# Optimization experiments

Measured on AMD Instinct MI355X. Metric: run time of the kernel, lower is better.

## Reference

```python
import jax, jax.numpy as jnp
import numpy as np

B, N_OBJ, N_REL = 32, 100, 512
D_OBJ, D_CTX, D_HID = 1024, 1024, 1024


def setup_inputs() -> dict:
    key = jax.random.key(0)
    k1, k2, k3, k4, k5 = jax.random.split(key, 5)
    object_branch_output = jax.random.normal(k1, (B * N_OBJ, D_OBJ), dtype=jnp.float32)
    context_branch_output = jax.random.normal(k2, (B, D_CTX), dtype=jnp.float32)
    num_obj = jnp.full((B,), N_OBJ, dtype=jnp.int32)
    num_rels = jnp.full((B,), N_REL, dtype=jnp.int32)
    obj_pairs = jax.random.randint(k3, (B, N_REL, 2), 0, N_OBJ, dtype=jnp.int32)
    W1 = jax.random.normal(k4, (D_OBJ + D_CTX, D_HID), dtype=jnp.float32) * (1.0 / np.sqrt(D_OBJ + D_CTX))
    b1 = jnp.zeros((D_HID,), dtype=jnp.float32)
    W2 = jax.random.normal(k5, (D_HID, D_HID), dtype=jnp.float32) * (1.0 / np.sqrt(D_HID))
    b2 = jnp.zeros((D_HID,), dtype=jnp.float32)
    return {
        "object_branch_output": object_branch_output,
        "context_branch_output": context_branch_output,
        "num_obj": num_obj,
        "num_rels": num_rels,
        "obj_pairs": obj_pairs,
        "W1": W1, "b1": b1, "W2": W2, "b2": b2,
    }


def reference(object_branch_output, context_branch_output, num_obj, num_rels,
              obj_pairs, W1, b1, W2, b2):
    # --- prepare_f_oo_vis_input, fully vectorized ---
    # per-batch object index offsets: sum(num_obj[:b])  (exclusive cumsum)
    obj_offsets = jnp.cumsum(num_obj) - num_obj                       # [B]
    global_pairs = obj_pairs + obj_offsets[:, None, None]             # [B, R, 2]
    # gather both endpoints of every pair and mean-aggregate
    pair_feats = object_branch_output[global_pairs]                   # [B, R, 2, D_obj]
    obj_vec = pair_feats.mean(axis=2)                                 # [B, R, D_obj]
    # broadcast per-batch context vector to every relation, then concat
    ctx = jnp.broadcast_to(context_branch_output[:, None, :],
                           obj_vec.shape[:2] + (context_branch_output.shape[-1],))
    input_f_oo_vis = jnp.concatenate([obj_vec, ctx], axis=-1)         # [B, R, D_obj+D_ctx]
    x = input_f_oo_vis.reshape(-1, input_f_oo_vis.shape[-1])          # [tot_rels, D_obj+D_ctx]
    # --- f_oo_vis MLP: (Linear -> ReLU) per layer pair ---
    h = jax.nn.relu(x @ W1 + b1)
    f_oo_vis_output = jax.nn.relu(h @ W2 + b2)
    return object_branch_output, f_oo_vis_output
```

## Files before the change

### kernel.cpp

```cpp
#include <hip/hip_runtime.h>
#include <hip/hip_bf16.h>

#define BB   32
#define NREL 512
#define DD   1024
#define MTOT (BB * NREL)
#define OBJ_ROWS (BB * 100)

typedef __attribute__((ext_vector_type(8))) short bf16x8;
typedef __attribute__((ext_vector_type(4))) float f32x4;

__device__ __forceinline__ unsigned short f2bf(float f) {
    union { float f; unsigned u; } v; v.f = f;
    unsigned r = v.u + 0x7fff + ((v.u >> 16) & 1);
    return (unsigned short)(r >> 16);
}

__device__ __forceinline__ void gld16(const void* g, void* l) {
    __builtin_amdgcn_global_load_lds(
        (const __attribute__((address_space(1))) unsigned int*)g,
        (__attribute__((address_space(3))) unsigned int*)l,
        16, 0, 0);
}

__device__ __forceinline__ void barfence() {
    asm volatile("" ::: "memory");
    __builtin_amdgcn_s_barrier();
    asm volatile("" ::: "memory");
}

__global__ void __launch_bounds__(256) prep_kernel(
    const float* __restrict__ obj, const float* __restrict__ ctx,
    const int* __restrict__ num_obj, const int* __restrict__ pairs,
    const float* __restrict__ W1, const float* __restrict__ W2,
    unsigned short* __restrict__ W1t, unsigned short* __restrict__ W2t,
    float* __restrict__ part, unsigned short* __restrict__ objvec,
    float* __restrict__ out_obj) {
    __shared__ float smem[32 * 33];
    int bid = blockIdx.x;
    int tid = threadIdx.x;

    if (bid < 1024) {
        int slice = bid & 3, chunk = (bid >> 2) & 7, b = bid >> 5;
        int nl = tid & 127, kh = tid >> 7;
        int n = chunk * 128 + nl;
        int kbase = slice * 256 + kh * 128;
        const float* c = ctx + (size_t)b * DD + kbase;
        const float* w = W1 + (size_t)(DD + kbase) * DD + n;
        float a0 = 0.f, a1 = 0.f, a2 = 0.f, a3 = 0.f;
#pragma unroll 8
        for (int k = 0; k < 128; k += 4) {
            a0 = fmaf(c[k + 0], w[(size_t)(k + 0) * DD], a0);
            a1 = fmaf(c[k + 1], w[(size_t)(k + 1) * DD], a1);
            a2 = fmaf(c[k + 2], w[(size_t)(k + 2) * DD], a2);
            a3 = fmaf(c[k + 3], w[(size_t)(k + 3) * DD], a3);
        }
        smem[kh * 128 + nl] = (a0 + a1) + (a2 + a3);
        __syncthreads();
        if (kh == 0)
            part[(((size_t)slice * BB + b) << 10) + n] = smem[nl] + smem[128 + nl];
    } else if (bid < 3072) {
        const float* W = (bid < 2048) ? W1 : W2;
        unsigned short* Wt = (bid < 2048) ? W1t : W2t;
        int t = (bid - 1024) & 1023;
        int k0 = (t >> 5) * 32, n0 = (t & 31) * 32;
        int tr = tid >> 5, tc = tid & 31;
#pragma unroll
        for (int i = 0; i < 4; i++)
            smem[(tr + i * 8) * 33 + tc] = W[(size_t)(k0 + tr + i * 8) * DD + n0 + tc];
        __syncthreads();
#pragma unroll
        for (int i = 0; i < 4; i++)
            Wt[(size_t)(n0 + tr + i * 8) * DD + k0 + tc] = f2bf(smem[tc * 33 + tr + i * 8]);
    } else if (bid < 7168) {
        int rbase = (bid - 3072) * 4;
        int b = rbase >> 9;
        int off = 0;
        for (int i = 0; i < b; i++) off += num_obj[i];
#pragma unroll
        for (int rr = 0; rr < 4; rr++) {
            int row = rbase + rr;
            int i0 = pairs[2 * row] + off;
            int i1 = pairs[2 * row + 1] + off;
            float4 x = ((const float4*)obj)[(size_t)i0 * (DD / 4) + tid];
            float4 y = ((const float4*)obj)[(size_t)i1 * (DD / 4) + tid];
            ushort4 o;
            o.x = f2bf(0.5f * (x.x + y.x));
            o.y = f2bf(0.5f * (x.y + y.y));
            o.z = f2bf(0.5f * (x.z + y.z));
            o.w = f2bf(0.5f * (x.w + y.w));
            ((ushort4*)(objvec + (size_t)row * DD))[tid] = o;
        }
    } else {
        const float4* src = (const float4*)obj;
        float4* dst = (float4*)out_obj;
        for (int i = (bid - 7168) * 256 + tid; i < OBJ_ROWS * DD / 4; i += 2048 * 256)
            dst[i] = src[i];
    }
}

template <int MODE>
__global__ void __launch_bounds__(512, 2) gemm256_kernel(
    const unsigned short* __restrict__ A,
    const unsigned short* __restrict__ Bt,
    const float* __restrict__ bias,
    const float* __restrict__ bias2,
    void* __restrict__ Cout) {
    constexpr int K = 1024;
    constexpr int NT = K / 64;
    extern __shared__ unsigned short lds[];
    int tid = threadIdx.x;
    int lane = tid & 63, wave = tid >> 6;
    int wr = wave >> 2, wc = wave & 3;
    int lr = lane & 15, g = lane >> 4;

    int wg = blockIdx.x;
    int swz = (wg & 7) * 32 + (wg >> 3);
    int mBase = (swz >> 2) * 256;
    int nBase = (swz & 3) * 256;

    const unsigned short* Ab = A + (size_t)mBase * K;
    const unsigned short* Bb = Bt + (size_t)nBase * K;

    int srow[4], soff[4], sdst[4];
#pragma unroll
    for (int i = 0; i < 4; i++) {
        int s = i * 512 + tid;
        int row = s >> 3, cperm = s & 7;
        srow[i] = row;
        soff[i] = (cperm ^ (row & 7)) * 8;
        sdst[i] = s * 8;
    }

    f32x4 acc[8][4];
#pragma unroll
    for (int i = 0; i < 8; i++)
#pragma unroll
        for (int j = 0; j < 4; j++) acc[i][j] = (f32x4){0.f, 0.f, 0.f, 0.f};

    auto STAGE = [&](int bi, int kt) {
        unsigned short* Ad = lds + bi * 16384;
        unsigned short* Bd = lds + 32768 + bi * 16384;
        int ko = kt * 64;
#pragma unroll
        for (int i = 0; i < 4; i++) {
            gld16(Ab + (size_t)srow[i] * K + ko + soff[i], Ad + sdst[i]);
            gld16(Bb + (size_t)srow[i] * K + ko + soff[i], Bd + sdst[i]);
        }
    };

    auto COMPUTE = [&](int bi) {
        const unsigned short* As = lds + bi * 16384;
        const unsigned short* Bs = lds + 32768 + bi * 16384;
        bf16x8 bfr[4][2];
#pragma unroll
        for (int n = 0; n < 4; n++)
#pragma unroll
            for (int kk = 0; kk < 2; kk++) {
                int row = wc * 64 + n * 16 + lr;
                int c = kk * 4 + g;
                bfr[n][kk] = *(const bf16x8*)&Bs[row * 64 + ((c ^ (row & 7)) * 8)];
            }
#pragma unroll
        for (int half = 0; half < 2; half++) {
            bf16x8 af[4][2];
#pragma unroll
            for (int m = 0; m < 4; m++)
#pragma unroll
                for (int kk = 0; kk < 2; kk++) {
                    int row = wr * 128 + (half * 4 + m) * 16 + lr;
                    int c = kk * 4 + g;
                    af[m][kk] = *(const bf16x8*)&As[row * 64 + ((c ^ (row & 7)) * 8)];
                }
            __builtin_amdgcn_s_setprio(1);
#pragma unroll
            for (int m = 0; m < 4; m++)
#pragma unroll
                for (int n = 0; n < 4; n++)
#pragma unroll
                    for (int kk = 0; kk < 2; kk++)
                        acc[half * 4 + m][n] = __builtin_amdgcn_mfma_f32_16x16x32_bf16(
                            af[m][kk], bfr[n][kk], acc[half * 4 + m][n], 0, 0, 0);
            __builtin_amdgcn_s_setprio(0);
        }
    };

    STAGE(0, 0);
    int cur = 0;
    for (int kt = 0; kt < NT - 1; ++kt) {
        STAGE(cur ^ 1, kt + 1);
        asm volatile("s_waitcnt vmcnt(8)" ::: "memory");
        barfence();
        COMPUTE(cur);
        barfence();
        cur ^= 1;
    }
    asm volatile("s_waitcnt vmcnt(0)" ::: "memory");
    barfence();
    COMPUTE(cur);

    int rg = g * 4;
    int bb = mBase >> 9;
#pragma unroll
    for (int m = 0; m < 8; m++) {
#pragma unroll
        for (int n = 0; n < 4; n++) {
            int col = nBase + wc * 64 + n * 16 + lr;
            float bv;
            if (MODE == 1) {
                bv = bias2[col];
#pragma unroll
                for (int s = 0; s < 4; s++)
                    bv += bias[(((size_t)s * BB + bb) << 10) + col];
            } else {
                bv = bias[col];
            }
#pragma unroll
            for (int r = 0; r < 4; r++) {
                int row = mBase + wr * 128 + m * 16 + rg + r;
                float v = acc[m][n][r] + bv;
                v = v > 0.f ? v : 0.f;
                if (MODE == 1)
                    ((unsigned short*)Cout)[(size_t)row * 1024 + col] = f2bf(v);
                else
                    ((float*)Cout)[(size_t)row * 1024 + col] = v;
            }
        }
    }
}

extern "C" void kernel_launch(void* const* d_in, const int* in_sizes, int n_in,
                              void* d_out, int out_size, void* d_ws, size_t ws_size,
                              hipStream_t stream) {
    (void)in_sizes; (void)n_in; (void)out_size; (void)ws_size;
    const float* obj     = (const float*)d_in[0];
    const float* ctx     = (const float*)d_in[1];
    const int*   num_obj = (const int*)d_in[2];
    const int*   pairs   = (const int*)d_in[4];
    const float* W1      = (const float*)d_in[5];
    const float* b1      = (const float*)d_in[6];
    const float* W2      = (const float*)d_in[7];
    const float* b2      = (const float*)d_in[8];

    char* ws = (char*)d_ws;
    unsigned short* objvec = (unsigned short*)(ws);
    unsigned short* h      = (unsigned short*)(ws + 33554432);
    unsigned short* W1t    = (unsigned short*)(ws + 67108864);
    unsigned short* W2t    = (unsigned short*)(ws + 69206016);

    float* out_obj = (float*)d_out;
    float* out_f   = out_obj + (size_t)OBJ_ROWS * DD;
    float* part    = out_f;

    hipFuncSetAttribute(reinterpret_cast<const void*>(gemm256_kernel<1>),
                        hipFuncAttributeMaxDynamicSharedMemorySize, 131072);
    hipFuncSetAttribute(reinterpret_cast<const void*>(gemm256_kernel<2>),
                        hipFuncAttributeMaxDynamicSharedMemorySize, 131072);

    prep_kernel<<<dim3(9216), 256, 0, stream>>>(
        obj, ctx, num_obj, pairs, W1, W2, W1t, W2t, part, objvec, out_obj);
    gemm256_kernel<1><<<dim3(256), 512, 131072, stream>>>(objvec, W1t, part, b1, (void*)h);
    gemm256_kernel<2><<<dim3(256), 512, 131072, stream>>>(h, W2t, b2, b2, (void*)out_f);
}
```

Measured before the change: 104.0 us.

## Apply W1 to object rows before gathering pairs to shrink first GEMM

```diff
diff --git a/kernel.cpp b/kernel.cpp
--- a/kernel.cpp
+++ b/kernel.cpp
@@ -16,6 +16,11 @@
     return (unsigned short)(r >> 16);
 }
 
+__device__ __forceinline__ float bf2f(unsigned short s) {
+    union { unsigned u; float f; } v; v.u = (unsigned)s << 16;
+    return v.f;
+}
+
 __device__ __forceinline__ void gld16(const void* g, void* l) {
     __builtin_amdgcn_global_load_lds(
         (const __attribute__((address_space(1))) unsigned int*)g,
@@ -31,10 +36,9 @@
 
 __global__ void __launch_bounds__(256) prep_kernel(
     const float* __restrict__ obj, const float* __restrict__ ctx,
-    const int* __restrict__ num_obj, const int* __restrict__ pairs,
     const float* __restrict__ W1, const float* __restrict__ W2,
     unsigned short* __restrict__ W1t, unsigned short* __restrict__ W2t,
-    float* __restrict__ part, unsigned short* __restrict__ objvec,
+    float* __restrict__ part, unsigned short* __restrict__ obj_bf,
     float* __restrict__ out_obj) {
     __shared__ float smem[32 * 33];
     int bid = blockIdx.x;
@@ -72,40 +76,123 @@
 #pragma unroll
         for (int i = 0; i < 4; i++)
             Wt[(size_t)(n0 + tr + i * 8) * DD + k0 + tc] = f2bf(smem[tc * 33 + tr + i * 8]);
-    } else if (bid < 7168) {
-        int rbase = (bid - 3072) * 4;
-        int b = rbase >> 9;
-        int off = 0;
-        for (int i = 0; i < b; i++) off += num_obj[i];
-#pragma unroll
-        for (int rr = 0; rr < 4; rr++) {
-            int row = rbase + rr;
-            int i0 = pairs[2 * row] + off;
-            int i1 = pairs[2 * row + 1] + off;
-            float4 x = ((const float4*)obj)[(size_t)i0 * (DD / 4) + tid];
-            float4 y = ((const float4*)obj)[(size_t)i1 * (DD / 4) + tid];
-            ushort4 o;
-            o.x = f2bf(0.5f * (x.x + y.x));
-            o.y = f2bf(0.5f * (x.y + y.y));
-            o.z = f2bf(0.5f * (x.z + y.z));
-            o.w = f2bf(0.5f * (x.w + y.w));
-            ((ushort4*)(objvec + (size_t)row * DD))[tid] = o;
-        }
     } else {
         const float4* src = (const float4*)obj;
         float4* dst = (float4*)out_obj;
-        for (int i = (bid - 7168) * 256 + tid; i < OBJ_ROWS * DD / 4; i += 2048 * 256)
-            dst[i] = src[i];
-    }
-}
-
-template <int MODE>
-__global__ void __launch_bounds__(512, 2) gemm256_kernel(
+        ushort4* dbf = (ushort4*)obj_bf;
+        for (int i = (bid - 3072) * 256 + tid; i < OBJ_ROWS * DD / 4; i += 2048 * 256) {
+            float4 v = src[i];
+            dst[i] = v;
+            ushort4 o;
+            o.x = f2bf(v.x); o.y = f2bf(v.y); o.z = f2bf(v.z); o.w = f2bf(v.w);
+            dbf[i] = o;
+        }
+    }
+}
+
+__global__ void __launch_bounds__(256) gemmP_kernel(
+    const unsigned short* __restrict__ A,
+    const unsigned short* __restrict__ Bt,
+    unsigned short* __restrict__ P) {
+    constexpr int K = 1024;
+    __shared__ __attribute__((aligned(16))) unsigned short As[128 * 32];
+    __shared__ __attribute__((aligned(16))) unsigned short Bs[128 * 32];
+    int tid = threadIdx.x;
+    int lane = tid & 63, wave = tid >> 6;
+    int wr = wave >> 1, wc = wave & 1;
+    int mBase = blockIdx.y * 128;
+    int nBase = blockIdx.x * 128;
+
+    f32x4 acc[4][4];
+#pragma unroll
+    for (int i = 0; i < 4; i++)
+#pragma unroll
+        for (int j = 0; j < 4; j++) acc[i][j] = (f32x4){0.f, 0.f, 0.f, 0.f};
+
+    const unsigned short* Ab = A + (size_t)mBase * K;
+    const unsigned short* Bb = Bt + (size_t)nBase * K;
+
+    for (int k0 = 0; k0 < K; k0 += 32) {
+#pragma unroll
+        for (int h = 0; h < 2; h++) {
+            int c = tid + h * 256;
+            int row = c >> 2, kc = (c & 3) * 8;
+            gld16(Ab + (size_t)row * K + k0 + kc, As + c * 8);
+            gld16(Bb + (size_t)row * K + k0 + kc, Bs + c * 8);
+        }
+        __syncthreads();
+        int lr = lane & 15, kg = (lane >> 4) * 8;
+        bf16x8 af[4], bfr[4];
+#pragma unroll
+        for (int m = 0; m < 4; m++)
+            af[m] = *(const bf16x8*)&As[(wr * 64 + m * 16 + lr) * 32 + kg];
+#pragma unroll
+        for (int n = 0; n < 4; n++)
+            bfr[n] = *(const bf16x8*)&Bs[(wc * 64 + n * 16 + lr) * 32 + kg];
+#pragma unroll
+        for (int m = 0; m < 4; m++)
+#pragma unroll
+            for (int n = 0; n < 4; n++)
+                acc[m][n] = __builtin_amdgcn_mfma_f32_16x16x32_bf16(af[m], bfr[n], acc[m][n], 0, 0, 0);
+        __syncthreads();
+    }
+
+    int lr = lane & 15, rg = (lane >> 4) * 4;
+#pragma unroll
+    for (int m = 0; m < 4; m++)
+#pragma unroll
+        for (int n = 0; n < 4; n++) {
+            int col = nBase + wc * 64 + n * 16 + lr;
+#pragma unroll
+            for (int r = 0; r < 4; r++) {
+                int row = mBase + wr * 64 + m * 16 + rg + r;
+                P[(size_t)row * DD + col] = f2bf(acc[m][n][r]);
+            }
+        }
+}
+
+__global__ void __launch_bounds__(256) hgen_kernel(
+    const unsigned short* __restrict__ P, const int* __restrict__ pairs,
+    const int* __restrict__ num_obj, const float* __restrict__ part,
+    const float* __restrict__ b1, unsigned short* __restrict__ h) {
+    int rbase = blockIdx.x * 4;
+    int b = rbase >> 9;
+    int off = 0;
+    for (int i = 0; i < b; i++) off += num_obj[i];
+    int t = threadIdx.x;
+
+    float4 bv = ((const float4*)b1)[t];
+#pragma unroll
+    for (int s = 0; s < 4; s++) {
+        float4 p = ((const float4*)(part + (((size_t)s * BB + b) << 10)))[t];
+        bv.x += p.x; bv.y += p.y; bv.z += p.z; bv.w += p.w;
+    }
+
+#pragma unroll
+    for (int rr = 0; rr < 4; rr++) {
+        int row = rbase + rr;
+        int i0 = pairs[2 * row] + off;
+        int i1 = pairs[2 * row + 1] + off;
+        ushort4 a = ((const ushort4*)(P + (size_t)i0 * DD))[t];
+        ushort4 c = ((const ushort4*)(P + (size_t)i1 * DD))[t];
+        float v0 = 0.5f * (bf2f(a.x) + bf2f(c.x)) + bv.x;
+        float v1 = 0.5f * (bf2f(a.y) + bf2f(c.y)) + bv.y;
+        float v2 = 0.5f * (bf2f(a.z) + bf2f(c.z)) + bv.z;
+        float v3 = 0.5f * (bf2f(a.w) + bf2f(c.w)) + bv.w;
+        ushort4 o;
+        o.x = f2bf(v0 > 0.f ? v0 : 0.f);
+        o.y = f2bf(v1 > 0.f ? v1 : 0.f);
+        o.z = f2bf(v2 > 0.f ? v2 : 0.f);
+        o.w = f2bf(v3 > 0.f ? v3 : 0.f);
+        ((ushort4*)(h + (size_t)row * DD))[t] = o;
+    }
+}
+
+__global__ void __launch_bounds__(512, 2) gemm2_kernel(
     const unsigned short* __restrict__ A,
     const unsigned short* __restrict__ Bt,
     const float* __restrict__ bias,
-    const float* __restrict__ bias2,
-    void* __restrict__ Cout) {
+    float* __restrict__ Cout) {
     constexpr int K = 1024;
     constexpr int NT = K / 64;
     extern __shared__ unsigned short lds[];
@@ -200,30 +287,17 @@
     COMPUTE(cur);
 
     int rg = g * 4;
-    int bb = mBase >> 9;
 #pragma unroll
     for (int m = 0; m < 8; m++) {
 #pragma unroll
         for (int n = 0; n < 4; n++) {
             int col = nBase + wc * 64 + n * 16 + lr;
-            float bv;
-            if (MODE == 1) {
-                bv = bias2[col];
-#pragma unroll
-                for (int s = 0; s < 4; s++)
-                    bv += bias[(((size_t)s * BB + bb) << 10) + col];
-            } else {
-                bv = bias[col];
-            }
+            float bv = bias[col];
 #pragma unroll
             for (int r = 0; r < 4; r++) {
                 int row = mBase + wr * 128 + m * 16 + rg + r;
                 float v = acc[m][n][r] + bv;
-                v = v > 0.f ? v : 0.f;
-                if (MODE == 1)
-                    ((unsigned short*)Cout)[(size_t)row * 1024 + col] = f2bf(v);
-                else
-                    ((float*)Cout)[(size_t)row * 1024 + col] = v;
+                Cout[(size_t)row * 1024 + col] = v > 0.f ? v : 0.f;
             }
         }
     }
@@ -243,22 +317,22 @@
     const float* b2      = (const float*)d_in[8];
 
     char* ws = (char*)d_ws;
-    unsigned short* objvec = (unsigned short*)(ws);
-    unsigned short* h      = (unsigned short*)(ws + 33554432);
-    unsigned short* W1t    = (unsigned short*)(ws + 67108864);
-    unsigned short* W2t    = (unsigned short*)(ws + 69206016);
+    unsigned short* obj_bf = (unsigned short*)(ws);
+    unsigned short* P      = (unsigned short*)(ws + 6553600);
+    unsigned short* h      = (unsigned short*)(ws + 13107200);
+    unsigned short* W1t    = (unsigned short*)(ws + 46661632);
+    unsigned short* W2t    = (unsigned short*)(ws + 48758784);
 
     float* out_obj = (float*)d_out;
     float* out_f   = out_obj + (size_t)OBJ_ROWS * DD;
     float* part    = out_f;
 
-    hipFuncSetAttribute(reinterpret_cast<const void*>(gemm256_kernel<1>),
+    hipFuncSetAttribute(reinterpret_cast<const void*>(gemm2_kernel),
                         hipFuncAttributeMaxDynamicSharedMemorySize, 131072);
-    hipFuncSetAttribute(reinterpret_cast<const void*>(gemm256_kernel<2>),
-                        hipFuncAttributeMaxDynamicSharedMemorySize, 131072);
-
-    prep_kernel<<<dim3(9216), 256, 0, stream>>>(
-        obj, ctx, num_obj, pairs, W1, W2, W1t, W2t, part, objvec, out_obj);
-    gemm256_kernel<1><<<dim3(256), 512, 131072, stream>>>(objvec, W1t, part, b1, (void*)h);
-    gemm256_kernel<2><<<dim3(256), 512, 131072, stream>>>(h, W2t, b2, b2, (void*)out_f);
-}
+
+    prep_kernel<<<dim3(5120), 256, 0, stream>>>(
+        obj, ctx, W1, W2, W1t, W2t, part, obj_bf, out_obj);
+    gemmP_kernel<<<dim3(8, 25), 256, 0, stream>>>(obj_bf, W1t, P);
+    hgen_kernel<<<dim3(4096), 256, 0, stream>>>(P, pairs, num_obj, part, b1, h);
+    gemm2_kernel<<<dim3(256), 512, 131072, stream>>>(h, W2t, b2, out_f);
+}
```

After: 90.50 us. 13.0% less time.
